# Kernel optimization log

Hardware: AMD Instinct MI355X
Metric: run time of the kernel (lower is better)

The kernel has to match this reference:

```python
import jax, jax.numpy as jnp
import numpy as np

N_NODES = 50000
N_EDGES = 800000
IN_DIM = 64
OUT_DIM = 64
HID = OUT_DIM // 2  # 32
N_LAYERS = 9  # layer_num; layer_num >= 7 => no temporal conv, conv dropout unused


def _layernorm(x, w, b, eps=1e-5):
    mu = jnp.mean(x, axis=-1, keepdims=True)
    var = jnp.var(x, axis=-1, keepdims=True)
    return (x - mu) * jax.lax.rsqrt(var + eps) * w + b


def _conv(x, Wp, Wn, Ws, src, tgt, pos_m, neg_m):
    # relation-wise gather -> linear -> masked merge -> single scatter_add
    xs = x[src]  # [E, d_in]
    m = jnp.where(pos_m[:, None], xs @ Wp.T, 0.0) + jnp.where(neg_m[:, None], xs @ Wn.T, 0.0)
    agg = jax.ops.segment_sum(m, tgt, num_segments=N_NODES)
    return agg + x @ Ws.T


def _asfr(x, ln_w, ln_b, gw, gb):
    xn = _layernorm(x, ln_w, ln_b)
    w = jax.nn.sigmoid(xn @ gw.T + gb)
    w1 = jnp.where(w > 0.5, 1.0, w)
    w2 = jnp.where(w > 0.5, 0.0, w)
    x1 = w1 * x
    x2 = w2 * x
    h = x.shape[1] // 2
    return jnp.concatenate([x1[:, :h] + x2[:, h:], x1[:, h:] + x2[:, :h]], axis=1)


def setup_inputs() -> dict:
    key = jax.random.key(0)
    ks = jax.random.split(key, 24)
    init_emb = jax.random.normal(ks[0], (N_NODES, IN_DIM), dtype=jnp.float32)
    src = jax.random.randint(ks[1], (N_EDGES,), 0, N_NODES)
    tgt = jax.random.randint(ks[2], (N_EDGES,), 0, N_NODES)
    sign = jnp.where(jax.random.uniform(ks[3], (N_EDGES,)) > 0.5, 1, -1).astype(jnp.int64)
    edge_index_s = jnp.stack([src, tgt, sign], axis=1).astype(jnp.int64)

    def w(k, shape, fan_in):
        return jax.random.normal(k, shape, dtype=jnp.float32) * (1.0 / np.sqrt(fan_in))

    inp = dict(init_emb=init_emb, edge_index_s=edge_index_s)
    # conv1: in 64 -> 32, relations pos/neg + self loop (no bias)
    inp["W1_pos"] = w(ks[4], (HID, IN_DIM), IN_DIM)
    inp["W1_neg"] = w(ks[5], (HID, IN_DIM), IN_DIM)
    inp["W1_self"] = w(ks[6], (HID, IN_DIM), IN_DIM)
    # 8 further convs: 32 -> 32, stacked
    L = N_LAYERS - 1
    inp["Wl_pos"] = w(ks[7], (L, HID, HID), HID)
    inp["Wl_neg"] = w(ks[8], (L, HID, HID), HID)
    inp["Wl_self"] = w(ks[9], (L, HID, HID), HID)
    # ASFR
    inp["asfr_ln_w"] = jnp.ones((HID,), jnp.float32)
    inp["asfr_ln_b"] = jnp.zeros((HID,), jnp.float32)
    inp["asfr_gate_w"] = w(ks[10], (HID, HID), HID)
    inp["asfr_gate_b"] = jnp.zeros((HID,), jnp.float32)
    # projection 32 -> 64
    inp["proj_w"] = w(ks[11], (OUT_DIM, HID), HID)
    inp["proj_b"] = jnp.zeros((OUT_DIM,), jnp.float32)
    # readout MLP: 64 -> 64 -> 64 -> 1, layernorm + relu between
    inp["mlp_w1"] = w(ks[12], (OUT_DIM, OUT_DIM), OUT_DIM)
    inp["mlp_b1"] = jnp.zeros((OUT_DIM,), jnp.float32)
    inp["mlp_ln1_w"] = jnp.ones((OUT_DIM,), jnp.float32)
    inp["mlp_ln1_b"] = jnp.zeros((OUT_DIM,), jnp.float32)
    inp["mlp_w2"] = w(ks[13], (OUT_DIM, OUT_DIM), OUT_DIM)
    inp["mlp_b2"] = jnp.zeros((OUT_DIM,), jnp.float32)
    inp["mlp_ln2_w"] = jnp.ones((OUT_DIM,), jnp.float32)
    inp["mlp_ln2_b"] = jnp.zeros((OUT_DIM,), jnp.float32)
    inp["mlp_w3"] = w(ks[14], (1, OUT_DIM), OUT_DIM)
    inp["mlp_b3"] = jnp.zeros((1,), jnp.float32)
    return inp


def reference(init_emb, edge_index_s, W1_pos, W1_neg, W1_self, Wl_pos, Wl_neg, Wl_self,
              asfr_ln_w, asfr_ln_b, asfr_gate_w, asfr_gate_b, proj_w, proj_b,
              mlp_w1, mlp_b1, mlp_ln1_w, mlp_ln1_b, mlp_w2, mlp_b2,
              mlp_ln2_w, mlp_ln2_b, mlp_w3, mlp_b3):
    src = edge_index_s[:, 0]
    tgt = edge_index_s[:, 1]
    sign = edge_index_s[:, 2]
    pos_m = sign > 0
    neg_m = sign < 0

    z = jax.nn.elu(_conv(init_emb, W1_pos, W1_neg, W1_self, src, tgt, pos_m, neg_m))
    z = _asfr(z, asfr_ln_w, asfr_ln_b, asfr_gate_w, asfr_gate_b)
    for i in range(Wl_pos.shape[0]):
        z_new = jax.nn.elu(_conv(z, Wl_pos[i], Wl_neg[i], Wl_self[i], src, tgt, pos_m, neg_m))
        z = z_new if i == 0 else z_new + 0.1 * z
    z = jax.nn.elu(z @ proj_w.T + proj_b)
    # readout MLP (eval mode: dropout identity)
    h = jax.nn.relu(_layernorm(z @ mlp_w1.T + mlp_b1, mlp_ln1_w, mlp_ln1_b))
    h = jax.nn.relu(_layernorm(h @ mlp_w2.T + mlp_b2, mlp_ln2_w, mlp_ln2_b))
    prob = jax.nn.sigmoid(h @ mlp_w3.T + mlp_b3)
    return (z, prob)
```

## Files before the change

kernel.cpp:

```cpp
#include <hip/hip_runtime.h>
#include <hip/hip_bf16.h>

#define NODES 50000
#define EDGES 800000
#define BSH 8
#define NBUCK 196
#define NBIN_BLOCKS 391

__device__ __forceinline__ float elu1(float x) { return x > 0.f ? x : expm1f(x); }

union F4 { float4 v; float f[4]; };

__global__ __launch_bounds__(256) void k_hist2(const int* __restrict__ ei, int* __restrict__ deg,
                                               int* __restrict__ bucket_cnt) {
  __shared__ int cnt[NBUCK];
  int t = threadIdx.x;
  for (int i = t; i < NBUCK; i += 256) cnt[i] = 0;
  __syncthreads();
  int base = blockIdx.x * 2048;
#pragma unroll
  for (int i = 0; i < 8; i++) {
    int e = base + i * 256 + t;
    if (e < EDGES) {
      int tgt = ei[e * 3 + 1];
      atomicAdd(deg + tgt, 1);
      atomicAdd(&cnt[tgt >> BSH], 1);
    }
  }
  __syncthreads();
  for (int i = t; i < NBUCK; i += 256)
    if (cnt[i]) atomicAdd(bucket_cnt + i, cnt[i]);
}

__global__ __launch_bounds__(512) void k_scan1(const int* __restrict__ deg, int* __restrict__ offs,
                                               int* __restrict__ bsum) {
  __shared__ int s[512];
  int t = threadIdx.x, i = blockIdx.x * 512 + t;
  int v = (i < NODES) ? deg[i] : 0;
  s[t] = v;
  __syncthreads();
  for (int o = 1; o < 512; o <<= 1) {
    int x = (t >= o) ? s[t - o] : 0;
    __syncthreads();
    s[t] += x;
    __syncthreads();
  }
  if (i < NODES) offs[i] = s[t] - v;
  if (t == 511) bsum[blockIdx.x] = s[511];
}

__global__ __launch_bounds__(128) void k_scan2(int* __restrict__ bsum, int nb) {
  __shared__ int s[128];
  int t = threadIdx.x;
  int v = (t < nb) ? bsum[t] : 0;
  s[t] = v;
  __syncthreads();
  for (int o = 1; o < 128; o <<= 1) {
    int x = (t >= o) ? s[t - o] : 0;
    __syncthreads();
    s[t] += x;
    __syncthreads();
  }
  if (t < nb) bsum[t] = s[t] - v;
}

__global__ __launch_bounds__(512) void k_scan3(int* __restrict__ offs, const int* __restrict__ bsum) {
  int i = blockIdx.x * 512 + threadIdx.x;
  if (i < NODES) offs[i] += bsum[blockIdx.x];
  if (i == 0) offs[NODES] = EDGES;
}

__global__ __launch_bounds__(256) void k_bscan(const int* __restrict__ bucket_cnt,
                                               int* __restrict__ bucket_base,
                                               int* __restrict__ bucket_cursor) {
  __shared__ int s[256];
  int t = threadIdx.x;
  int v = (t < NBUCK) ? bucket_cnt[t] : 0;
  s[t] = v;
  __syncthreads();
  for (int o = 1; o < 256; o <<= 1) {
    int x = (t >= o) ? s[t - o] : 0;
    __syncthreads();
    s[t] += x;
    __syncthreads();
  }
  if (t < NBUCK) { int e = s[t] - v; bucket_base[t] = e; bucket_cursor[t] = e; }
}

__global__ __launch_bounds__(256) void k_bin(const int* __restrict__ ei,
                                             int* __restrict__ bucket_cursor,
                                             uint2* __restrict__ binned) {
  __shared__ int cnt[NBUCK], base[NBUCK];
  int t = threadIdx.x;
  for (int i = t; i < NBUCK; i += 256) cnt[i] = 0;
  __syncthreads();
  int eb = blockIdx.x * 2048;
#pragma unroll
  for (int i = 0; i < 8; i++) {
    int e = eb + i * 256 + t;
    if (e < EDGES) atomicAdd(&cnt[ei[e * 3 + 1] >> BSH], 1);
  }
  __syncthreads();
  for (int i = t; i < NBUCK; i += 256) {
    int c = cnt[i];
    base[i] = c ? atomicAdd(bucket_cursor + i, c) : 0;
    cnt[i] = 0;
  }
  __syncthreads();
#pragma unroll
  for (int i = 0; i < 8; i++) {
    int e = eb + i * 256 + t;
    if (e < EDGES) {
      int src = ei[e * 3 + 0];
      int tgt = ei[e * 3 + 1];
      int sg  = ei[e * 3 + 2];
      unsigned val = (unsigned)src | (sg < 0 ? 0x80000000u : 0u);
      int bkt = tgt >> BSH;
      int r = atomicAdd(&cnt[bkt], 1);
      binned[base[bkt] + r] = make_uint2(val, (unsigned)tgt);
    }
  }
}

__global__ __launch_bounds__(256) void k_scatter2(const uint2* __restrict__ binned,
                                                  const int* __restrict__ bucket_base,
                                                  const int* __restrict__ bucket_cnt,
                                                  const int* __restrict__ offs,
                                                  unsigned* __restrict__ perm) {
  __shared__ int cur[256];
  int b = blockIdx.x, t = threadIdx.x;
  int t0 = b << BSH;
  cur[t] = (t0 + t < NODES) ? offs[t0 + t] : 0;
  __syncthreads();
  int n = bucket_cnt[b], bb = bucket_base[b];
  for (int i = t; i < n; i += 256) {
    uint2 e = binned[bb + i];
    int p = atomicAdd(&cur[e.y - t0], 1);
    perm[p] = e.x;
  }
}

__global__ __launch_bounds__(256) void k_lin64(const float* __restrict__ x,
    const float* __restrict__ Wp, const float* __restrict__ Wn, const float* __restrict__ Ws,
    __hip_bfloat16* __restrict__ ypb, __hip_bfloat16* __restrict__ ynb, float* __restrict__ ys) {
  constexpr int K4 = 16;
  __shared__ float4 wp[K4][32], wn[K4][32], wsm[K4][32];
  __shared__ float4 xs[8][K4];
  for (int i = threadIdx.x; i < 32 * K4; i += 256) {
    int k4 = i >> 5, c = i & 31;
    wp[k4][c]  = ((const float4*)Wp)[c * K4 + k4];
    wn[k4][c]  = ((const float4*)Wn)[c * K4 + k4];
    wsm[k4][c] = ((const float4*)Ws)[c * K4 + k4];
  }
  int base = blockIdx.x * 8;
  for (int i = threadIdx.x; i < 8 * K4; i += 256) {
    int r = i / K4, k4 = i - r * K4;
    xs[r][k4] = ((const float4*)(x + (size_t)(base + r) * 64))[k4];
  }
  __syncthreads();
  int lane = threadIdx.x & 31, local = threadIdx.x >> 5;
  float ap = 0.f, an = 0.f, asf = 0.f;
#pragma unroll
  for (int k4 = 0; k4 < K4; k4++) {
    float4 xv = xs[local][k4];
    float4 a = wp[k4][lane], b = wn[k4][lane], c = wsm[k4][lane];
    ap  = fmaf(xv.w, a.w, fmaf(xv.z, a.z, fmaf(xv.y, a.y, fmaf(xv.x, a.x, ap))));
    an  = fmaf(xv.w, b.w, fmaf(xv.z, b.z, fmaf(xv.y, b.y, fmaf(xv.x, b.x, an))));
    asf = fmaf(xv.w, c.w, fmaf(xv.z, c.z, fmaf(xv.y, c.y, fmaf(xv.x, c.x, asf))));
  }
  size_t o = (size_t)(base + local) * 32 + lane;
  ypb[o] = __float2bfloat16(ap);
  ynb[o] = __float2bfloat16(an);
  ys[o] = asf;
}

#define ACC8(A, V)                                   \
  A[0] += __uint_as_float((V).x << 16);              \
  A[1] += __uint_as_float((V).x & 0xffff0000u);      \
  A[2] += __uint_as_float((V).y << 16);              \
  A[3] += __uint_as_float((V).y & 0xffff0000u);      \
  A[4] += __uint_as_float((V).z << 16);              \
  A[5] += __uint_as_float((V).z & 0xffff0000u);      \
  A[6] += __uint_as_float((V).w << 16);              \
  A[7] += __uint_as_float((V).w & 0xffff0000u);

template <int DO_ASFR, int DO_RES, int DO_LIN, int WRITE_Z>
__global__ __launch_bounds__(256) void k_layer(
    const unsigned short* __restrict__ ypi, const unsigned short* __restrict__ yni,
    float* __restrict__ ys,
    const unsigned* __restrict__ perm, const int* __restrict__ offs,
    float* __restrict__ z,
    const float* __restrict__ lnw, const float* __restrict__ lnb,
    const float* __restrict__ gw, const float* __restrict__ gb,
    const float* __restrict__ Wp, const float* __restrict__ Wn, const float* __restrict__ Ws,
    __hip_bfloat16* __restrict__ ypo, __hip_bfloat16* __restrict__ yno) {
  __shared__ float4 wps[8][32], wns[8][32], wss[8][32], gws[8][32];
  __shared__ float zrow[8][36], xrow[8][36];
  int t = threadIdx.x;
  if (DO_LIN) {
    int k4 = t >> 5, c = t & 31;
    wps[k4][c] = ((const float4*)Wp)[c * 8 + k4];
    wns[k4][c] = ((const float4*)Wn)[c * 8 + k4];
    wss[k4][c] = ((const float4*)Ws)[c * 8 + k4];
    if (DO_ASFR) gws[k4][c] = ((const float4*)gw)[c * 8 + k4];
  }
  int lane = t & 31, local = t >> 5;
  int node = blockIdx.x * 8 + local;
  int es = lane >> 2, fs = lane & 3;
  int beg = offs[node], end = offs[node + 1];
  float a0[8], a1[8];
#pragma unroll
  for (int i = 0; i < 8; i++) { a0[i] = 0.f; a1[i] = 0.f; }
  int b = beg + es;
  for (; b + 8 < end; b += 16) {
    unsigned u0 = perm[b];
    unsigned u1 = perm[b + 8];
    const unsigned short* p0 = (u0 >> 31) ? yni : ypi;
    const unsigned short* p1 = (u1 >> 31) ? yni : ypi;
    uint4 v0 = *((const uint4*)(p0 + (size_t)(u0 & 0x7FFFFFFFu) * 32) + fs);
    uint4 v1 = *((const uint4*)(p1 + (size_t)(u1 & 0x7FFFFFFFu) * 32) + fs);
    ACC8(a0, v0);
    ACC8(a1, v1);
  }
  if (b < end) {
    unsigned u0 = perm[b];
    const unsigned short* p0 = (u0 >> 31) ? yni : ypi;
    uint4 v0 = *((const uint4*)(p0 + (size_t)(u0 & 0x7FFFFFFFu) * 32) + fs);
    ACC8(a0, v0);
  }
#pragma unroll
  for (int i = 0; i < 8; i++) a0[i] += a1[i];
#pragma unroll
  for (int m = 4; m <= 16; m <<= 1) {
#pragma unroll
    for (int i = 0; i < 8; i++) a0[i] += __shfl_xor(a0[i], m, 32);
  }
  if (es == 0) {
    const float* ysr = ys + (size_t)node * 32 + fs * 8;
    F4 s0, s1;
    s0.v = *(const float4*)ysr;
    s1.v = *(const float4*)(ysr + 4);
    float o[8];
#pragma unroll
    for (int i = 0; i < 4; i++) o[i] = elu1(a0[i] + s0.f[i]);
#pragma unroll
    for (int i = 0; i < 4; i++) o[4 + i] = elu1(a0[4 + i] + s1.f[i]);
    if (DO_RES) {
      const float* rr = z + (size_t)node * 32 + fs * 8;
      F4 r0, r1;
      r0.v = *(const float4*)rr;
      r1.v = *(const float4*)(rr + 4);
#pragma unroll
      for (int i = 0; i < 4; i++) { o[i] += 0.1f * r0.f[i]; o[4 + i] += 0.1f * r1.f[i]; }
    }
#pragma unroll
    for (int i = 0; i < 8; i++) zrow[local][fs * 8 + i] = o[i];
    if (WRITE_Z) {
      float* zw = z + (size_t)node * 32 + fs * 8;
      *(float4*)zw = make_float4(o[0], o[1], o[2], o[3]);
      *(float4*)(zw + 4) = make_float4(o[4], o[5], o[6], o[7]);
    }
  }
  __syncthreads();
  if (!DO_LIN) return;
  if (DO_ASFR) {
    float v = zrow[local][lane];
    float s = v;
#pragma unroll
    for (int m = 16; m; m >>= 1) s += __shfl_xor(s, m, 32);
    float mu = s * (1.f / 32.f);
    float d = v - mu, sq = d * d;
#pragma unroll
    for (int m = 16; m; m >>= 1) sq += __shfl_xor(sq, m, 32);
    float xn = d * rsqrtf(sq * (1.f / 32.f) + 1e-5f) * lnw[lane] + lnb[lane];
    xrow[local][lane] = xn;
    float ga = gb[lane];
#pragma unroll
    for (int k4 = 0; k4 < 8; k4++) {
      float4 xv = *((const float4*)&xrow[local][0] + k4);
      float4 w = gws[k4][lane];
      ga = fmaf(xv.w, w.w, fmaf(xv.z, w.z, fmaf(xv.y, w.y, fmaf(xv.x, w.x, ga))));
    }
    float g = 1.f / (1.f + __expf(-ga));
    float w1 = g > 0.5f ? 1.f : g;
    float w2 = g > 0.5f ? 0.f : g;
    float zn = w1 * v + __shfl_xor(w2 * v, 16, 32);
    zrow[local][lane] = zn;
  }
  float ap = 0.f, an = 0.f, asf = 0.f;
#pragma unroll
  for (int k4 = 0; k4 < 8; k4++) {
    float4 xv = *((const float4*)&zrow[local][0] + k4);
    float4 a2 = wps[k4][lane], b2 = wns[k4][lane], c2 = wss[k4][lane];
    ap  = fmaf(xv.w, a2.w, fmaf(xv.z, a2.z, fmaf(xv.y, a2.y, fmaf(xv.x, a2.x, ap))));
    an  = fmaf(xv.w, b2.w, fmaf(xv.z, b2.z, fmaf(xv.y, b2.y, fmaf(xv.x, b2.x, an))));
    asf = fmaf(xv.w, c2.w, fmaf(xv.z, c2.z, fmaf(xv.y, c2.y, fmaf(xv.x, c2.x, asf))));
  }
  size_t o = (size_t)node * 32 + lane;
  ypo[o] = __float2bfloat16(ap);
  yno[o] = __float2bfloat16(an);
  ys[o] = asf;
}

__global__ __launch_bounds__(256) void k_mlp(const float* __restrict__ z,
    const float* __restrict__ pw, const float* __restrict__ pb,
    const float* __restrict__ w1, const float* __restrict__ b1,
    const float* __restrict__ l1w, const float* __restrict__ l1b,
    const float* __restrict__ w2, const float* __restrict__ b2,
    const float* __restrict__ l2w, const float* __restrict__ l2b,
    const float* __restrict__ w3, const float* __restrict__ b3,
    float* __restrict__ outz, float* __restrict__ outp) {
  __shared__ float4 pT4[32 * 16];
  __shared__ float4 w1T4[64 * 16], w2T4[64 * 16];
  __shared__ float4 hbuf4[64 * 17];
  __shared__ float pb_s[64], b1_s[64], l1w_s[64], l1b_s[64], b2_s[64], l2w_s[64], l2b_s[64], w3_s[64];
  int t = threadIdx.x;
  for (int i = t; i < 512; i += 256) {
    int k = i >> 4, j4 = i & 15;
    float4 v;
    v.x = pw[(j4 * 4 + 0) * 32 + k]; v.y = pw[(j4 * 4 + 1) * 32 + k];
    v.z = pw[(j4 * 4 + 2) * 32 + k]; v.w = pw[(j4 * 4 + 3) * 32 + k];
    pT4[i] = v;
  }
  for (int i = t; i < 1024; i += 256) {
    int k = i >> 4, j4 = i & 15;
    float4 v, u;
    v.x = w1[(j4 * 4 + 0) * 64 + k]; v.y = w1[(j4 * 4 + 1) * 64 + k];
    v.z = w1[(j4 * 4 + 2) * 64 + k]; v.w = w1[(j4 * 4 + 3) * 64 + k];
    u.x = w2[(j4 * 4 + 0) * 64 + k]; u.y = w2[(j4 * 4 + 1) * 64 + k];
    u.z = w2[(j4 * 4 + 2) * 64 + k]; u.w = w2[(j4 * 4 + 3) * 64 + k];
    w1T4[i] = v; w2T4[i] = u;
  }
  if (t < 64) {
    pb_s[t] = pb[t]; b1_s[t] = b1[t]; l1w_s[t] = l1w[t]; l1b_s[t] = l1b[t];
    b2_s[t] = b2[t]; l2w_s[t] = l2w[t]; l2b_s[t] = l2b[t]; w3_s[t] = w3[t];
  }
  __syncthreads();
  int g = t >> 2, q = t & 3;
  int node = blockIdx.x * 64 + g;
  if (node >= NODES) return;
  float bb3 = b3[0];
  {
    const float4* z4 = (const float4*)(z + (size_t)node * 32);
    hbuf4[g * 17 + q * 2 + 0] = z4[q * 2 + 0];
    hbuf4[g * 17 + q * 2 + 1] = z4[q * 2 + 1];
  }
  float acc[16], h[16];
#pragma unroll
  for (int i = 0; i < 16; i++) acc[i] = pb_s[q * 16 + i];
#pragma unroll 2
  for (int k4 = 0; k4 < 8; k4++) {
    F4 hv; hv.v = hbuf4[g * 17 + k4];
#pragma unroll
    for (int c = 0; c < 4; c++) {
      float hk = hv.f[c];
      const float4* wrow = &pT4[(k4 * 4 + c) * 16 + q * 4];
#pragma unroll
      for (int j4 = 0; j4 < 4; j4++) {
        float4 w = wrow[j4];
        acc[j4 * 4 + 0] = fmaf(hk, w.x, acc[j4 * 4 + 0]);
        acc[j4 * 4 + 1] = fmaf(hk, w.y, acc[j4 * 4 + 1]);
        acc[j4 * 4 + 2] = fmaf(hk, w.z, acc[j4 * 4 + 2]);
        acc[j4 * 4 + 3] = fmaf(hk, w.w, acc[j4 * 4 + 3]);
      }
    }
  }
#pragma unroll
  for (int i = 0; i < 16; i++) h[i] = elu1(acc[i]);
  {
    float4* oz = (float4*)(outz + (size_t)node * 64 + q * 16);
#pragma unroll
    for (int i4 = 0; i4 < 4; i4++)
      oz[i4] = make_float4(h[i4 * 4], h[i4 * 4 + 1], h[i4 * 4 + 2], h[i4 * 4 + 3]);
#pragma unroll
    for (int i4 = 0; i4 < 4; i4++)
      hbuf4[g * 17 + q * 4 + i4] = make_float4(h[i4 * 4], h[i4 * 4 + 1], h[i4 * 4 + 2], h[i4 * 4 + 3]);
  }
#pragma unroll
  for (int i = 0; i < 16; i++) acc[i] = b1_s[q * 16 + i];
#pragma unroll 2
  for (int k4 = 0; k4 < 16; k4++) {
    F4 hv; hv.v = hbuf4[g * 17 + k4];
#pragma unroll
    for (int c = 0; c < 4; c++) {
      float hk = hv.f[c];
      const float4* wrow = &w1T4[(k4 * 4 + c) * 16 + q * 4];
#pragma unroll
      for (int j4 = 0; j4 < 4; j4++) {
        float4 w = wrow[j4];
        acc[j4 * 4 + 0] = fmaf(hk, w.x, acc[j4 * 4 + 0]);
        acc[j4 * 4 + 1] = fmaf(hk, w.y, acc[j4 * 4 + 1]);
        acc[j4 * 4 + 2] = fmaf(hk, w.z, acc[j4 * 4 + 2]);
        acc[j4 * 4 + 3] = fmaf(hk, w.w, acc[j4 * 4 + 3]);
      }
    }
  }
  {
    float s = 0.f;
#pragma unroll
    for (int i = 0; i < 16; i++) s += acc[i];
    s += __shfl_xor(s, 1, 4); s += __shfl_xor(s, 2, 4);
    float mu = s * (1.f / 64.f);
    float vs = 0.f;
#pragma unroll
    for (int i = 0; i < 16; i++) { float dd = acc[i] - mu; vs += dd * dd; }
    vs += __shfl_xor(vs, 1, 4); vs += __shfl_xor(vs, 2, 4);
    float rs = rsqrtf(vs * (1.f / 64.f) + 1e-5f);
#pragma unroll
    for (int i = 0; i < 16; i++)
      h[i] = fmaxf((acc[i] - mu) * rs * l1w_s[q * 16 + i] + l1b_s[q * 16 + i], 0.f);
  }
#pragma unroll
  for (int i4 = 0; i4 < 4; i4++)
    hbuf4[g * 17 + q * 4 + i4] = make_float4(h[i4 * 4], h[i4 * 4 + 1], h[i4 * 4 + 2], h[i4 * 4 + 3]);
#pragma unroll
  for (int i = 0; i < 16; i++) acc[i] = b2_s[q * 16 + i];
#pragma unroll 2
  for (int k4 = 0; k4 < 16; k4++) {
    F4 hv; hv.v = hbuf4[g * 17 + k4];
#pragma unroll
    for (int c = 0; c < 4; c++) {
      float hk = hv.f[c];
      const float4* wrow = &w2T4[(k4 * 4 + c) * 16 + q * 4];
#pragma unroll
      for (int j4 = 0; j4 < 4; j4++) {
        float4 w = wrow[j4];
        acc[j4 * 4 + 0] = fmaf(hk, w.x, acc[j4 * 4 + 0]);
        acc[j4 * 4 + 1] = fmaf(hk, w.y, acc[j4 * 4 + 1]);
        acc[j4 * 4 + 2] = fmaf(hk, w.z, acc[j4 * 4 + 2]);
        acc[j4 * 4 + 3] = fmaf(hk, w.w, acc[j4 * 4 + 3]);
      }
    }
  }
  {
    float s = 0.f;
#pragma unroll
    for (int i = 0; i < 16; i++) s += acc[i];
    s += __shfl_xor(s, 1, 4); s += __shfl_xor(s, 2, 4);
    float mu = s * (1.f / 64.f);
    float vs = 0.f;
#pragma unroll
    for (int i = 0; i < 16; i++) { float dd = acc[i] - mu; vs += dd * dd; }
    vs += __shfl_xor(vs, 1, 4); vs += __shfl_xor(vs, 2, 4);
    float rs = rsqrtf(vs * (1.f / 64.f) + 1e-5f);
    float p = 0.f;
#pragma unroll
    for (int i = 0; i < 16; i++) {
      float hv2 = fmaxf((acc[i] - mu) * rs * l2w_s[q * 16 + i] + l2b_s[q * 16 + i], 0.f);
      p = fmaf(hv2, w3_s[q * 16 + i], p);
    }
    p += __shfl_xor(p, 1, 4); p += __shfl_xor(p, 2, 4);
    if (q == 0) outp[node] = 1.f / (1.f + __expf(-(p + bb3)));
  }
}

extern "C" void kernel_launch(void* const* d_in, const int* in_sizes, int n_in,
                              void* d_out, int out_size, void* d_ws, size_t ws_size,
                              hipStream_t stream) {
  const float* init_emb = (const float*)d_in[0];
  const int*   ei  = (const int*)d_in[1];
  const float* W1p = (const float*)d_in[2];
  const float* W1n = (const float*)d_in[3];
  const float* W1s = (const float*)d_in[4];
  const float* Wlp = (const float*)d_in[5];
  const float* Wln = (const float*)d_in[6];
  const float* Wls = (const float*)d_in[7];
  const float* lnw = (const float*)d_in[8];
  const float* lnb = (const float*)d_in[9];
  const float* gw  = (const float*)d_in[10];
  const float* gb  = (const float*)d_in[11];
  const float* pw  = (const float*)d_in[12];
  const float* pb  = (const float*)d_in[13];
  const float* w1  = (const float*)d_in[14];
  const float* b1  = (const float*)d_in[15];
  const float* l1w = (const float*)d_in[16];
  const float* l1b = (const float*)d_in[17];
  const float* w2  = (const float*)d_in[18];
  const float* b2  = (const float*)d_in[19];
  const float* l2w = (const float*)d_in[20];
  const float* l2b = (const float*)d_in[21];
  const float* w3  = (const float*)d_in[22];
  const float* b3  = (const float*)d_in[23];

  char* ws = (char*)d_ws;
  size_t off = 0;
  auto alloc = [&](size_t b) { void* p = ws + off; off = (off + b + 255) & ~(size_t)255; return p; };
  __hip_bfloat16* ypA = (__hip_bfloat16*)alloc(NODES * 32 * 2);
  __hip_bfloat16* ynA = (__hip_bfloat16*)alloc(NODES * 32 * 2);
  __hip_bfloat16* ypB = (__hip_bfloat16*)alloc(NODES * 32 * 2);
  __hip_bfloat16* ynB = (__hip_bfloat16*)alloc(NODES * 32 * 2);
  float*    ysel   = (float*)alloc(NODES * 32 * 4);
  float*    zbuf   = (float*)alloc(NODES * 32 * 4);
  unsigned* perm   = (unsigned*)alloc(EDGES * 4);
  int*      deg    = (int*)alloc(NODES * 4);
  int*      offs   = (int*)alloc((NODES + 1) * 4);
  int*      bsum   = (int*)alloc(128 * 4);
  int*      bucket_cnt    = (int*)alloc(NBUCK * 4);
  int*      bucket_base   = (int*)alloc(NBUCK * 4);
  int*      bucket_cursor = (int*)alloc(NBUCK * 4);
  uint2*    binned = (uint2*)ypA;

  hipMemsetAsync(deg, 0, NODES * 4, stream);
  hipMemsetAsync(bucket_cnt, 0, NBUCK * 4, stream);
  k_hist2<<<NBIN_BLOCKS, 256, 0, stream>>>(ei, deg, bucket_cnt);
  int nb = (NODES + 511) / 512;
  k_scan1<<<nb, 512, 0, stream>>>(deg, offs, bsum);
  k_scan2<<<1, 128, 0, stream>>>(bsum, nb);
  k_scan3<<<nb, 512, 0, stream>>>(offs, bsum);
  k_bscan<<<1, 256, 0, stream>>>(bucket_cnt, bucket_base, bucket_cursor);
  k_bin<<<NBIN_BLOCKS, 256, 0, stream>>>(ei, bucket_cursor, binned);
  k_scatter2<<<NBUCK, 256, 0, stream>>>(binned, bucket_base, bucket_cnt, offs, perm);

  const int G = NODES / 8;
  k_lin64<<<G, 256, 0, stream>>>(init_emb, W1p, W1n, W1s, ypA, ynA, ysel);
  k_layer<1, 0, 1, 0><<<G, 256, 0, stream>>>((const unsigned short*)ypA, (const unsigned short*)ynA,
      ysel, perm, offs, zbuf, lnw, lnb, gw, gb, Wlp, Wln, Wls, ypB, ynB);
  k_layer<0, 0, 1, 1><<<G, 256, 0, stream>>>((const unsigned short*)ypB, (const unsigned short*)ynB,
      ysel, perm, offs, zbuf, nullptr, nullptr, nullptr, nullptr,
      Wlp + 1024, Wln + 1024, Wls + 1024, ypA, ynA);
  const __hip_bfloat16* yin_p = ypA; const __hip_bfloat16* yin_n = ynA;
  __hip_bfloat16* yout_p = ypB; __hip_bfloat16* yout_n = ynB;
  for (int i = 1; i < 7; i++) {
    k_layer<0, 1, 1, 1><<<G, 256, 0, stream>>>((const unsigned short*)yin_p, (const unsigned short*)yin_n,
        ysel, perm, offs, zbuf, nullptr, nullptr, nullptr, nullptr,
        Wlp + (i + 1) * 1024, Wln + (i + 1) * 1024, Wls + (i + 1) * 1024, yout_p, yout_n);
    const __hip_bfloat16* tp = yin_p; const __hip_bfloat16* tn = yin_n;
    yin_p = yout_p; yin_n = yout_n;
    yout_p = (__hip_bfloat16*)tp; yout_n = (__hip_bfloat16*)tn;
  }
  k_layer<0, 1, 0, 1><<<G, 256, 0, stream>>>((const unsigned short*)yin_p, (const unsigned short*)yin_n,
      ysel, perm, offs, zbuf, nullptr, nullptr, nullptr, nullptr,
      nullptr, nullptr, nullptr, nullptr, nullptr);

  float* outz = (float*)d_out;
  float* outp = outz + (size_t)NODES * 64;
  k_mlp<<<(NODES * 4 + 255) / 256, 256, 0, stream>>>(zbuf, pw, pb, w1, b1, l1w, l1b,
                                                     w2, b2, l2w, l2b, w3, b3, outz, outp);
}
```

Measured before the change: 395.7 us.

## Aggregate bf16 z per sign then apply weights, replacing pre-projected pos/neg gathers

Layers 2-9 no longer pre-project z into separate bf16 pos/neg buffers. Each layer gathers a single bf16 copy of z per edge, accumulates it into separate positive and negative sums, and applies Wp/Wn/Ws to the aggregated rows afterwards. This uses linearity so one buffer is written per layer instead of two bf16 buffers plus the fp32 self term. The MLP kernel also replaces shared-memory staging of hidden rows with intra-quad shuffles. The cost is doubled accumulator registers and shuffle reductions in the gather loop, plus extra rounding from keeping z in bf16.

Result: slower. 494.2 us (+24.9%).

```diff
diff --git a/kernel.cpp b/kernel.cpp
--- a/kernel.cpp
+++ b/kernel.cpp
@@ -184,25 +184,36 @@
   A[6] += __uint_as_float((V).w << 16);              \
   A[7] += __uint_as_float((V).w & 0xffff0000u);
 
-template <int DO_ASFR, int DO_RES, int DO_LIN, int WRITE_Z>
-__global__ __launch_bounds__(256) void k_layer(
+__device__ __forceinline__ void accPN(float* accP, float* accN, uint4 v, bool neg) {
+  float f[8];
+  f[0] = __uint_as_float(v.x << 16);
+  f[1] = __uint_as_float(v.x & 0xffff0000u);
+  f[2] = __uint_as_float(v.y << 16);
+  f[3] = __uint_as_float(v.y & 0xffff0000u);
+  f[4] = __uint_as_float(v.z << 16);
+  f[5] = __uint_as_float(v.z & 0xffff0000u);
+  f[6] = __uint_as_float(v.w << 16);
+  f[7] = __uint_as_float(v.w & 0xffff0000u);
+#pragma unroll
+  for (int i = 0; i < 8; i++) {
+    accP[i] += neg ? 0.f : f[i];
+    accN[i] += neg ? f[i] : 0.f;
+  }
+}
+
+__global__ __launch_bounds__(256) void k_layer0(
     const unsigned short* __restrict__ ypi, const unsigned short* __restrict__ yni,
-    float* __restrict__ ys,
+    const float* __restrict__ ys,
     const unsigned* __restrict__ perm, const int* __restrict__ offs,
-    float* __restrict__ z,
     const float* __restrict__ lnw, const float* __restrict__ lnb,
     const float* __restrict__ gw, const float* __restrict__ gb,
-    const float* __restrict__ Wp, const float* __restrict__ Wn, const float* __restrict__ Ws,
-    __hip_bfloat16* __restrict__ ypo, __hip_bfloat16* __restrict__ yno) {
-  __shared__ float4 wps[8][32], wns[8][32], wss[8][32], gws[8][32];
+    float* __restrict__ zbuf, __hip_bfloat16* __restrict__ zb16) {
+  __shared__ float4 gws[8][32];
   __shared__ float zrow[8][36], xrow[8][36];
   int t = threadIdx.x;
-  if (DO_LIN) {
+  {
     int k4 = t >> 5, c = t & 31;
-    wps[k4][c] = ((const float4*)Wp)[c * 8 + k4];
-    wns[k4][c] = ((const float4*)Wn)[c * 8 + k4];
-    wss[k4][c] = ((const float4*)Ws)[c * 8 + k4];
-    if (DO_ASFR) gws[k4][c] = ((const float4*)gw)[c * 8 + k4];
+    gws[k4][c] = ((const float4*)gw)[c * 8 + k4];
   }
   int lane = t & 31, local = t >> 5;
   int node = blockIdx.x * 8 + local;
@@ -240,66 +251,109 @@
     F4 s0, s1;
     s0.v = *(const float4*)ysr;
     s1.v = *(const float4*)(ysr + 4);
-    float o[8];
-#pragma unroll
-    for (int i = 0; i < 4; i++) o[i] = elu1(a0[i] + s0.f[i]);
-#pragma unroll
-    for (int i = 0; i < 4; i++) o[4 + i] = elu1(a0[4 + i] + s1.f[i]);
-    if (DO_RES) {
-      const float* rr = z + (size_t)node * 32 + fs * 8;
-      F4 r0, r1;
-      r0.v = *(const float4*)rr;
-      r1.v = *(const float4*)(rr + 4);
-#pragma unroll
-      for (int i = 0; i < 4; i++) { o[i] += 0.1f * r0.f[i]; o[4 + i] += 0.1f * r1.f[i]; }
-    }
-#pragma unroll
-    for (int i = 0; i < 8; i++) zrow[local][fs * 8 + i] = o[i];
-    if (WRITE_Z) {
-      float* zw = z + (size_t)node * 32 + fs * 8;
-      *(float4*)zw = make_float4(o[0], o[1], o[2], o[3]);
-      *(float4*)(zw + 4) = make_float4(o[4], o[5], o[6], o[7]);
-    }
-  }
-  __syncthreads();
-  if (!DO_LIN) return;
-  if (DO_ASFR) {
-    float v = zrow[local][lane];
-    float s = v;
-#pragma unroll
-    for (int m = 16; m; m >>= 1) s += __shfl_xor(s, m, 32);
-    float mu = s * (1.f / 32.f);
-    float d = v - mu, sq = d * d;
-#pragma unroll
-    for (int m = 16; m; m >>= 1) sq += __shfl_xor(sq, m, 32);
-    float xn = d * rsqrtf(sq * (1.f / 32.f) + 1e-5f) * lnw[lane] + lnb[lane];
-    xrow[local][lane] = xn;
-    float ga = gb[lane];
-#pragma unroll
-    for (int k4 = 0; k4 < 8; k4++) {
-      float4 xv = *((const float4*)&xrow[local][0] + k4);
-      float4 w = gws[k4][lane];
-      ga = fmaf(xv.w, w.w, fmaf(xv.z, w.z, fmaf(xv.y, w.y, fmaf(xv.x, w.x, ga))));
-    }
-    float g = 1.f / (1.f + __expf(-ga));
-    float w1 = g > 0.5f ? 1.f : g;
-    float w2 = g > 0.5f ? 0.f : g;
-    float zn = w1 * v + __shfl_xor(w2 * v, 16, 32);
-    zrow[local][lane] = zn;
-  }
-  float ap = 0.f, an = 0.f, asf = 0.f;
+#pragma unroll
+    for (int i = 0; i < 4; i++) zrow[local][fs * 8 + i] = elu1(a0[i] + s0.f[i]);
+#pragma unroll
+    for (int i = 0; i < 4; i++) zrow[local][fs * 8 + 4 + i] = elu1(a0[4 + i] + s1.f[i]);
+  }
+  __syncthreads();
+  float v = zrow[local][lane];
+  float s = v;
+#pragma unroll
+  for (int m = 16; m; m >>= 1) s += __shfl_xor(s, m, 32);
+  float mu = s * (1.f / 32.f);
+  float d = v - mu, sq = d * d;
+#pragma unroll
+  for (int m = 16; m; m >>= 1) sq += __shfl_xor(sq, m, 32);
+  float xn = d * rsqrtf(sq * (1.f / 32.f) + 1e-5f) * lnw[lane] + lnb[lane];
+  xrow[local][lane] = xn;
+  float ga = gb[lane];
 #pragma unroll
   for (int k4 = 0; k4 < 8; k4++) {
-    float4 xv = *((const float4*)&zrow[local][0] + k4);
+    float4 xv = *((const float4*)&xrow[local][0] + k4);
+    float4 w = gws[k4][lane];
+    ga = fmaf(xv.w, w.w, fmaf(xv.z, w.z, fmaf(xv.y, w.y, fmaf(xv.x, w.x, ga))));
+  }
+  float g = 1.f / (1.f + __expf(-ga));
+  float w1 = g > 0.5f ? 1.f : g;
+  float w2 = g > 0.5f ? 0.f : g;
+  float zn = w1 * v + __shfl_xor(w2 * v, 16, 32);
+  size_t o = (size_t)node * 32 + lane;
+  zbuf[o] = zn;
+  zb16[o] = __float2bfloat16(zn);
+}
+
+template <int DO_RES, int WRITE_B16>
+__global__ __launch_bounds__(256) void k_layerZ(
+    const unsigned short* __restrict__ zin16,
+    const unsigned* __restrict__ perm, const int* __restrict__ offs,
+    float* __restrict__ zbuf,
+    const float* __restrict__ Wp, const float* __restrict__ Wn, const float* __restrict__ Ws,
+    __hip_bfloat16* __restrict__ zout16) {
+  __shared__ float4 wps[8][32], wns[8][32], wss[8][32];
+  __shared__ float aprow[8][36], anrow[8][36], znrow[8][36];
+  int t = threadIdx.x;
+  {
+    int k4 = t >> 5, c = t & 31;
+    wps[k4][c] = ((const float4*)Wp)[c * 8 + k4];
+    wns[k4][c] = ((const float4*)Wn)[c * 8 + k4];
+    wss[k4][c] = ((const float4*)Ws)[c * 8 + k4];
+  }
+  int lane = t & 31, local = t >> 5;
+  int node = blockIdx.x * 8 + local;
+  int es = lane >> 2, fs = lane & 3;
+  float zv = zbuf[(size_t)node * 32 + lane];
+  znrow[local][lane] = zv;
+  int beg = offs[node], end = offs[node + 1];
+  float accP[8], accN[8];
+#pragma unroll
+  for (int i = 0; i < 8; i++) { accP[i] = 0.f; accN[i] = 0.f; }
+  int b = beg + es;
+  for (; b + 8 < end; b += 16) {
+    unsigned u0 = perm[b];
+    unsigned u1 = perm[b + 8];
+    uint4 v0 = *((const uint4*)(zin16 + (size_t)(u0 & 0x7FFFFFFFu) * 32) + fs);
+    uint4 v1 = *((const uint4*)(zin16 + (size_t)(u1 & 0x7FFFFFFFu) * 32) + fs);
+    accPN(accP, accN, v0, u0 >> 31);
+    accPN(accP, accN, v1, u1 >> 31);
+  }
+  if (b < end) {
+    unsigned u0 = perm[b];
+    uint4 v0 = *((const uint4*)(zin16 + (size_t)(u0 & 0x7FFFFFFFu) * 32) + fs);
+    accPN(accP, accN, v0, u0 >> 31);
+  }
+#pragma unroll
+  for (int m = 4; m <= 16; m <<= 1) {
+#pragma unroll
+    for (int i = 0; i < 8; i++) {
+      accP[i] += __shfl_xor(accP[i], m, 32);
+      accN[i] += __shfl_xor(accN[i], m, 32);
+    }
+  }
+  if (es == 0) {
+#pragma unroll
+    for (int i = 0; i < 8; i++) {
+      aprow[local][fs * 8 + i] = accP[i];
+      anrow[local][fs * 8 + i] = accN[i];
+    }
+  }
+  __syncthreads();
+  float m = 0.f;
+#pragma unroll
+  for (int k4 = 0; k4 < 8; k4++) {
+    float4 ap = *((const float4*)&aprow[local][0] + k4);
+    float4 an = *((const float4*)&anrow[local][0] + k4);
+    float4 zn = *((const float4*)&znrow[local][0] + k4);
     float4 a2 = wps[k4][lane], b2 = wns[k4][lane], c2 = wss[k4][lane];
-    ap  = fmaf(xv.w, a2.w, fmaf(xv.z, a2.z, fmaf(xv.y, a2.y, fmaf(xv.x, a2.x, ap))));
-    an  = fmaf(xv.w, b2.w, fmaf(xv.z, b2.z, fmaf(xv.y, b2.y, fmaf(xv.x, b2.x, an))));
-    asf = fmaf(xv.w, c2.w, fmaf(xv.z, c2.z, fmaf(xv.y, c2.y, fmaf(xv.x, c2.x, asf))));
-  }
+    m = fmaf(ap.w, a2.w, fmaf(ap.z, a2.z, fmaf(ap.y, a2.y, fmaf(ap.x, a2.x, m))));
+    m = fmaf(an.w, b2.w, fmaf(an.z, b2.z, fmaf(an.y, b2.y, fmaf(an.x, b2.x, m))));
+    m = fmaf(zn.w, c2.w, fmaf(zn.z, c2.z, fmaf(zn.y, c2.y, fmaf(zn.x, c2.x, m))));
+  }
+  float znew = elu1(m);
+  if (DO_RES) znew += 0.1f * zv;
   size_t o = (size_t)node * 32 + lane;
-  ypo[o] = __float2bfloat16(ap);
-  yno[o] = __float2bfloat16(an);
-  ys[o] = asf;
+  zbuf[o] = znew;
+  if (WRITE_B16) zout16[o] = __float2bfloat16(znew);
 }
 
 __global__ __launch_bounds__(256) void k_mlp(const float* __restrict__ z,
@@ -312,7 +366,6 @@
     float* __restrict__ outz, float* __restrict__ outp) {
   __shared__ float4 pT4[32 * 16];
   __shared__ float4 w1T4[64 * 16], w2T4[64 * 16];
-  __shared__ float4 hbuf4[64 * 17];
   __shared__ float pb_s[64], b1_s[64], l1w_s[64], l1b_s[64], b2_s[64], l2w_s[64], l2b_s[64], w3_s[64];
   int t = threadIdx.x;
   for (int i = t; i < 512; i += 256) {
@@ -340,29 +393,28 @@
   int node = blockIdx.x * 64 + g;
   if (node >= NODES) return;
   float bb3 = b3[0];
+  float xr[8];
   {
     const float4* z4 = (const float4*)(z + (size_t)node * 32);
-    hbuf4[g * 17 + q * 2 + 0] = z4[q * 2 + 0];
-    hbuf4[g * 17 + q * 2 + 1] = z4[q * 2 + 1];
+    F4 a, b;
+    a.v = z4[q * 2]; b.v = z4[q * 2 + 1];
+#pragma unroll
+    for (int i = 0; i < 4; i++) { xr[i] = a.f[i]; xr[4 + i] = b.f[i]; }
   }
   float acc[16], h[16];
 #pragma unroll
   for (int i = 0; i < 16; i++) acc[i] = pb_s[q * 16 + i];
-#pragma unroll 2
-  for (int k4 = 0; k4 < 8; k4++) {
-    F4 hv; hv.v = hbuf4[g * 17 + k4];
-#pragma unroll
-    for (int c = 0; c < 4; c++) {
-      float hk = hv.f[c];
-      const float4* wrow = &pT4[(k4 * 4 + c) * 16 + q * 4];
-#pragma unroll
-      for (int j4 = 0; j4 < 4; j4++) {
-        float4 w = wrow[j4];
-        acc[j4 * 4 + 0] = fmaf(hk, w.x, acc[j4 * 4 + 0]);
-        acc[j4 * 4 + 1] = fmaf(hk, w.y, acc[j4 * 4 + 1]);
-        acc[j4 * 4 + 2] = fmaf(hk, w.z, acc[j4 * 4 + 2]);
-        acc[j4 * 4 + 3] = fmaf(hk, w.w, acc[j4 * 4 + 3]);
-      }
+#pragma unroll
+  for (int k = 0; k < 32; k++) {
+    float hk = __shfl(xr[k & 7], k >> 3, 4);
+    const float4* wrow = &pT4[k * 16 + q * 4];
+#pragma unroll
+    for (int j4 = 0; j4 < 4; j4++) {
+      float4 w = wrow[j4];
+      acc[j4 * 4 + 0] = fmaf(hk, w.x, acc[j4 * 4 + 0]);
+      acc[j4 * 4 + 1] = fmaf(hk, w.y, acc[j4 * 4 + 1]);
+      acc[j4 * 4 + 2] = fmaf(hk, w.z, acc[j4 * 4 + 2]);
+      acc[j4 * 4 + 3] = fmaf(hk, w.w, acc[j4 * 4 + 3]);
     }
   }
 #pragma unroll
@@ -372,27 +424,20 @@
 #pragma unroll
     for (int i4 = 0; i4 < 4; i4++)
       oz[i4] = make_float4(h[i4 * 4], h[i4 * 4 + 1], h[i4 * 4 + 2], h[i4 * 4 + 3]);
-#pragma unroll
-    for (int i4 = 0; i4 < 4; i4++)
-      hbuf4[g * 17 + q * 4 + i4] = make_float4(h[i4 * 4], h[i4 * 4 + 1], h[i4 * 4 + 2], h[i4 * 4 + 3]);
   }
 #pragma unroll
   for (int i = 0; i < 16; i++) acc[i] = b1_s[q * 16 + i];
-#pragma unroll 2
-  for (int k4 = 0; k4 < 16; k4++) {
-    F4 hv; hv.v = hbuf4[g * 17 + k4];
-#pragma unroll
-    for (int c = 0; c < 4; c++) {
-      float hk = hv.f[c];
-      const float4* wrow = &w1T4[(k4 * 4 + c) * 16 + q * 4];
-#pragma unroll
-      for (int j4 = 0; j4 < 4; j4++) {
-        float4 w = wrow[j4];
-        acc[j4 * 4 + 0] = fmaf(hk, w.x, acc[j4 * 4 + 0]);
-        acc[j4 * 4 + 1] = fmaf(hk, w.y, acc[j4 * 4 + 1]);
-        acc[j4 * 4 + 2] = fmaf(hk, w.z, acc[j4 * 4 + 2]);
-        acc[j4 * 4 + 3] = fmaf(hk, w.w, acc[j4 * 4 + 3]);
-      }
+#pragma unroll
+  for (int k = 0; k < 64; k++) {
+    float hk = __shfl(h[k & 15], k >> 4, 4);
+    const float4* wrow = &w1T4[k * 16 + q * 4];
+#pragma unroll
+    for (int j4 = 0; j4 < 4; j4++) {
+      float4 w = wrow[j4];
+      acc[j4 * 4 + 0] = fmaf(hk, w.x, acc[j4 * 4 + 0]);
+      acc[j4 * 4 + 1] = fmaf(hk, w.y, acc[j4 * 4 + 1]);
+      acc[j4 * 4 + 2] = fmaf(hk, w.z, acc[j4 * 4 + 2]);
+      acc[j4 * 4 + 3] = fmaf(hk, w.w, acc[j4 * 4 + 3]);
     }
   }
   {
@@ -411,25 +456,18 @@
       h[i] = fmaxf((acc[i] - mu) * rs * l1w_s[q * 16 + i] + l1b_s[q * 16 + i], 0.f);
   }
 #pragma unroll
-  for (int i4 = 0; i4 < 4; i4++)
-    hbuf4[g * 17 + q * 4 + i4] = make_float4(h[i4 * 4], h[i4 * 4 + 1], h[i4 * 4 + 2], h[i4 * 4 + 3]);
-#pragma unroll
   for (int i = 0; i < 16; i++) acc[i] = b2_s[q * 16 + i];
-#pragma unroll 2
-  for (int k4 = 0; k4 < 16; k4++) {
-    F4 hv; hv.v = hbuf4[g * 17 + k4];
-#pragma unroll
-    for (int c = 0; c < 4; c++) {
-      float hk = hv.f[c];
-      const float4* wrow = &w2T4[(k4 * 4 + c) * 16 + q * 4];
-#pragma unroll
-      for (int j4 = 0; j4 < 4; j4++) {
-        float4 w = wrow[j4];
-        acc[j4 * 4 + 0] = fmaf(hk, w.x, acc[j4 * 4 + 0]);
-        acc[j4 * 4 + 1] = fmaf(hk, w.y, acc[j4 * 4 + 1]);
-        acc[j4 * 4 + 2] = fmaf(hk, w.z, acc[j4 * 4 + 2]);
-        acc[j4 * 4 + 3] = fmaf(hk, w.w, acc[j4 * 4 + 3]);
-      }
+#pragma unroll
+  for (int k = 0; k < 64; k++) {
+    float hk = __shfl(h[k & 15], k >> 4, 4);
+    const float4* wrow = &w2T4[k * 16 + q * 4];
+#pragma unroll
+    for (int j4 = 0; j4 < 4; j4++) {
+      float4 w = wrow[j4];
+      acc[j4 * 4 + 0] = fmaf(hk, w.x, acc[j4 * 4 + 0]);
+      acc[j4 * 4 + 1] = fmaf(hk, w.y, acc[j4 * 4 + 1]);
+      acc[j4 * 4 + 2] = fmaf(hk, w.z, acc[j4 * 4 + 2]);
+      acc[j4 * 4 + 3] = fmaf(hk, w.w, acc[j4 * 4 + 3]);
     }
   }
   {
@@ -487,10 +525,10 @@
   auto alloc = [&](size_t b) { void* p = ws + off; off = (off + b + 255) & ~(size_t)255; return p; };
   __hip_bfloat16* ypA = (__hip_bfloat16*)alloc(NODES * 32 * 2);
   __hip_bfloat16* ynA = (__hip_bfloat16*)alloc(NODES * 32 * 2);
-  __hip_bfloat16* ypB = (__hip_bfloat16*)alloc(NODES * 32 * 2);
-  __hip_bfloat16* ynB = (__hip_bfloat16*)alloc(NODES * 32 * 2);
   float*    ysel   = (float*)alloc(NODES * 32 * 4);
   float*    zbuf   = (float*)alloc(NODES * 32 * 4);
+  __hip_bfloat16* zbA = (__hip_bfloat16*)alloc(NODES * 32 * 2);
+  __hip_bfloat16* zbB = (__hip_bfloat16*)alloc(NODES * 32 * 2);
   unsigned* perm   = (unsigned*)alloc(EDGES * 4);
   int*      deg    = (int*)alloc(NODES * 4);
   int*      offs   = (int*)alloc((NODES + 1) * 4);
@@ -513,24 +551,21 @@
 
   const int G = NODES / 8;
   k_lin64<<<G, 256, 0, stream>>>(init_emb, W1p, W1n, W1s, ypA, ynA, ysel);
-  k_layer<1, 0, 1, 0><<<G, 256, 0, stream>>>((const unsigned short*)ypA, (const unsigned short*)ynA,
-      ysel, perm, offs, zbuf, lnw, lnb, gw, gb, Wlp, Wln, Wls, ypB, ynB);
-  k_layer<0, 0, 1, 1><<<G, 256, 0, stream>>>((const unsigned short*)ypB, (const unsigned short*)ynB,
-      ysel, perm, offs, zbuf, nullptr, nullptr, nullptr, nullptr,
-      Wlp + 1024, Wln + 1024, Wls + 1024, ypA, ynA);
-  const __hip_bfloat16* yin_p = ypA; const __hip_bfloat16* yin_n = ynA;
-  __hip_bfloat16* yout_p = ypB; __hip_bfloat16* yout_n = ynB;
+  k_layer0<<<G, 256, 0, stream>>>((const unsigned short*)ypA, (const unsigned short*)ynA,
+                                  ysel, perm, offs, lnw, lnb, gw, gb, zbuf, zbA);
+  k_layerZ<0, 1><<<G, 256, 0, stream>>>((const unsigned short*)zbA, perm, offs, zbuf,
+                                        Wlp, Wln, Wls, zbB);
+  const __hip_bfloat16* zin = zbB;
+  __hip_bfloat16* zout = zbA;
   for (int i = 1; i < 7; i++) {
-    k_layer<0, 1, 1, 1><<<G, 256, 0, stream>>>((const unsigned short*)yin_p, (const unsigned short*)yin_n,
-        ysel, perm, offs, zbuf, nullptr, nullptr, nullptr, nullptr,
-        Wlp + (i + 1) * 1024, Wln + (i + 1) * 1024, Wls + (i + 1) * 1024, yout_p, yout_n);
-    const __hip_bfloat16* tp = yin_p; const __hip_bfloat16* tn = yin_n;
-    yin_p = yout_p; yin_n = yout_n;
-    yout_p = (__hip_bfloat16*)tp; yout_n = (__hip_bfloat16*)tn;
-  }
-  k_layer<0, 1, 0, 1><<<G, 256, 0, stream>>>((const unsigned short*)yin_p, (const unsigned short*)yin_n,
-      ysel, perm, offs, zbuf, nullptr, nullptr, nullptr, nullptr,
-      nullptr, nullptr, nullptr, nullptr, nullptr);
+    k_layerZ<1, 1><<<G, 256, 0, stream>>>((const unsigned short*)zin, perm, offs, zbuf,
+                                          Wlp + i * 1024, Wln + i * 1024, Wls + i * 1024, zout);
+    const __hip_bfloat16* tp = zin;
+    zin = zout;
+    zout = (__hip_bfloat16*)tp;
+  }
+  k_layerZ<1, 0><<<G, 256, 0, stream>>>((const unsigned short*)zin, perm, offs, zbuf,
+                                        Wlp + 7 * 1024, Wln + 7 * 1024, Wls + 7 * 1024, nullptr);
 
   float* outz = (float*)d_out;
   float* outp = outz + (size_t)NODES * 64;
```
